# Kernel tuning notes

Measured on AMD Instinct MI355X. Metric: run time of the kernel, lower is better.

Reference implementation:

```python
import jax, jax.numpy as jnp
import numpy as np

VOCAB = 50000
EMB = 300
HID = 1024
MAXLEN = 128
BATCH = 256
M2 = 512


def _xavier(k, shape):
    lim = np.sqrt(6.0 / (shape[0] + shape[-1]))
    return jax.random.uniform(k, shape, jnp.float32, -lim, lim)


def setup_inputs() -> dict:
    key = jax.random.key(0)
    ks = jax.random.split(key, 16)
    return {
        "input1": jax.random.randint(ks[0], (BATCH, MAXLEN), 0, VOCAB, dtype=jnp.int32),
        "input2": jax.random.randint(ks[1], (BATCH, MAXLEN), 0, VOCAB, dtype=jnp.int32),
        "seqlen1": jax.random.randint(ks[2], (BATCH,), 1, MAXLEN + 1, dtype=jnp.int32),
        "seqlen2": jax.random.randint(ks[3], (BATCH,), 1, MAXLEN + 1, dtype=jnp.int32),
        "embeddings": jax.random.normal(ks[4], (VOCAB, EMB), jnp.float32) * 0.1,
        "lstm_kernel": _xavier(ks[5], (EMB + HID, 4 * HID)),
        "lstm_bias": jnp.zeros((4 * HID,), jnp.float32),
        "c1_init": _xavier(ks[6], (BATCH, HID)),
        "h1_init": _xavier(ks[7], (BATCH, HID)),
        "c2_init": _xavier(ks[8], (BATCH, HID)),
        "h2_init": _xavier(ks[9], (BATCH, HID)),
        "W_h": _xavier(ks[10], (HID + 1, HID + 1)),
        "W1": _xavier(ks[11], (3 * (HID + 1) + 1 + BATCH, M2)),
        "b1": _xavier(ks[12], (1, M2)),
        "W2": _xavier(ks[13], (M2, 2)),
        "b2": _xavier(ks[14], (1, 2)),
    }


def _lstm_last_state(x, seqlen, c0, h0, kernel, bias):
    # TF BasicLSTMCell: gates in order i, j, f, o; forget_bias=1.0.
    # dynamic_rnn(sequence_length=...) freezes state past each row's seqlen.
    E = x.shape[-1]
    Wx, Wh = kernel[:E], kernel[E:]
    xg = jnp.einsum('bte,eg->btg', x, Wx) + bias  # [B,T,4H], input proj hoisted out of scan
    T = x.shape[1]

    def step(carry, inputs):
        c, h = carry
        xg_t, t = inputs
        g = xg_t + h @ Wh
        i, j, f, o = jnp.split(g, 4, axis=-1)
        c_new = jax.nn.sigmoid(f + 1.0) * c + jax.nn.sigmoid(i) * jnp.tanh(j)
        h_new = jnp.tanh(c_new) * jax.nn.sigmoid(o)
        valid = (t < seqlen)[:, None]
        return (jnp.where(valid, c_new, c), jnp.where(valid, h_new, h)), None

    (c, h), _ = jax.lax.scan(step, (c0, h0), (jnp.swapaxes(xg, 0, 1), jnp.arange(T)))
    return h


def reference(input1, input2, seqlen1, seqlen2, embeddings, lstm_kernel, lstm_bias,
              c1_init, h1_init, c2_init, h2_init, W_h, W1, b1, W2, b2):
    x1 = embeddings[input1]  # [B,T,E]
    x2 = embeddings[input2]
    h1 = _lstm_last_state(x1, seqlen1, c1_init, h1_init, lstm_kernel, lstm_bias)
    h2 = _lstm_last_state(x2, seqlen2, c2_init, h2_init, lstm_kernel, lstm_bias)
    len1 = (seqlen1.astype(jnp.float32) / float(MAXLEN))[:, None]
    len2 = (seqlen2.astype(jnp.float32) / float(MAXLEN))[:, None]
    h1 = jnp.concatenate([h1, len1], axis=1)  # [B,H+1]
    h2 = jnp.concatenate([h2, len2], axis=1)
    h_dist = jnp.sum(jnp.square(h1 - h2), axis=1, keepdims=True)  # [B,1]
    h_mul = h1 * h2                                               # [B,H+1]
    h_interaction = (h1 @ W_h) @ h2.T                             # [B,B] bilinear block
    h_combined = jnp.concatenate([h1, h2, h_dist, h_mul, h_interaction], axis=1)
    e1 = jax.nn.relu(h_combined @ W1 + b1)  # dropout keep_prob=1 at inference -> identity
    return e1 @ W2 + b2  # [B,2] logits
```

## Files before the change

kernel.cpp:

```cpp
#include <hip/hip_runtime.h>
#include <hip/hip_bf16.h>

typedef __bf16 bf16;
typedef __bf16 bf16x8 __attribute__((ext_vector_type(8)));
typedef float f32x4 __attribute__((ext_vector_type(4)));

#define N_ROWS   512
#define HID      1024
#define KX       320
#define KTOT     1344
#define NSTEPS   128
#define EMB_D    300
#define HC_W     3332

#define WBT_OFF   0UL
#define XB_OFF    11010048UL
#define HB_OFF    52953088UL
#define BIASP_OFF 55050240UL
#define CB_OFF    55066624UL
#define HC_OFF    11010048UL
#define H2T_OFF   14422016UL
#define T1A_OFF   15471616UL
#define T1B_OFF   16521216UL
#define E1A_OFF   17570816UL
#define E1B_OFF   18095104UL


__device__ __forceinline__ float sigm(float x) { return 1.f / (1.f + __expf(-x)); }
__device__ __forceinline__ float tanh_fast(float x) {
  float xc = fminf(fmaxf(x, -15.f), 15.f);
  float e = __expf(2.f * xc);
  return (e - 1.f) / (e + 1.f);
}

__device__ __forceinline__ void lds_barrier() {
  asm volatile("s_waitcnt lgkmcnt(0)" ::: "memory");
  __builtin_amdgcn_sched_barrier(0);
  __builtin_amdgcn_s_barrier();
  __builtin_amdgcn_sched_barrier(0);
}

__global__ void pack_wbt(const float* __restrict__ lk, bf16* __restrict__ wbt) {
  __shared__ float sh[64][65];
  const int px = blockIdx.x;
  const int k0 = blockIdx.y * 64;
  const int t = threadIdx.x;
  {
    const int kk = t >> 2, g = t & 3;
    const int k = k0 + kk;
    const bool valid = (k < KX) ? (k < EMB_D) : true;
    const int src = (k < KX) ? k : (k - 20);
    const float* base = lk + (size_t)src * 4096 + g * 1024 + px * 16;
#pragma unroll
    for (int c4 = 0; c4 < 4; ++c4) {
      float4 v = valid ? *reinterpret_cast<const float4*>(base + c4 * 4)
                       : float4{0.f, 0.f, 0.f, 0.f};
      sh[kk][g * 16 + c4 * 4 + 0] = v.x;
      sh[kk][g * 16 + c4 * 4 + 1] = v.y;
      sh[kk][g * 16 + c4 * 4 + 2] = v.z;
      sh[kk][g * 16 + c4 * 4 + 3] = v.w;
    }
  }
  __syncthreads();
  {
    const int pl = t >> 2, kq = (t & 3) * 16;
    bf16 ov[16];
#pragma unroll
    for (int j = 0; j < 16; ++j) ov[j] = (bf16)sh[kq + j][pl];
    bf16* dst = wbt + (size_t)(px * 64 + pl) * KTOT + k0 + kq;
#pragma unroll
    for (int j = 0; j < 2; ++j)
      *reinterpret_cast<bf16x8*>(dst + j * 8) =
          *reinterpret_cast<const bf16x8*>(&ov[j * 8]);
  }
}

__global__ void pack_xb(const int* __restrict__ in1, const int* __restrict__ in2,
                        const float* __restrict__ emb, bf16* __restrict__ xb) {
  int r = blockIdx.x;
  int t = blockIdx.y * 8 + threadIdx.x / 40;
  int e8 = threadIdx.x % 40;
  int tok = (r < 256) ? in1[r * 128 + t] : in2[(r - 256) * 128 + t];
  const float* er = emb + (size_t)tok * EMB_D + e8 * 8;
  bf16x8 v;
  if (e8 < 37) {
#pragma unroll
    for (int i = 0; i < 8; ++i) v[i] = (bf16)er[i];
  } else {
#pragma unroll
    for (int i = 0; i < 8; ++i) {
      int e = e8 * 8 + i;
      v[i] = (e < EMB_D) ? (bf16)er[i] : (bf16)0.f;
    }
  }
  *reinterpret_cast<bf16x8*>(&xb[((size_t)t * N_ROWS + r) * KX + e8 * 8]) = v;
}

__global__ void pack_misc(const float* __restrict__ h1i, const float* __restrict__ h2i,
                          const float* __restrict__ c1i, const float* __restrict__ c2i,
                          const float* __restrict__ bias, bf16* __restrict__ hb0,
                          float* __restrict__ biasp, float* __restrict__ Cb) {
  int idx = blockIdx.x * 256 + threadIdx.x;
  if (idx < N_ROWS * HID) {
    int r = idx >> 10, k = idx & 1023;
    float v = (r < 256) ? h1i[(size_t)r * HID + k] : h2i[(size_t)(r - 256) * HID + k];
    hb0[idx] = (bf16)v;
    float cv = (r < 256) ? c1i[(size_t)r * HID + k] : c2i[(size_t)(r - 256) * HID + k];
    Cb[idx] = cv;
  }
  if (idx < 4096) {
    int cb = idx >> 6, g = (idx >> 4) & 3, c = idx & 15;
    biasp[idx] = bias[g * HID + cb * 16 + c];
  }
}

__launch_bounds__(256, 2)
__global__ void lstm_step(const bf16* __restrict__ xb, const bf16* __restrict__ wbt,
                          bf16* __restrict__ hb, const float* __restrict__ biasp,
                          float* __restrict__ Cb, const int* __restrict__ s1,
                          const int* __restrict__ s2, int t) {
  __shared__ bf16 As[2][128][64];
  __shared__ bf16 Bs[2][64][64];
  const int tid = threadIdx.x;
  const int wave = tid >> 6;
  const int lane = tid & 63;
  const int lrow = lane & 15;
  const int hi = lane >> 4;
  const int l7 = lane & 7;
  const int bid = blockIdx.x;
  const int rb = bid >> 6;
  const int cb = bid & 63;
  const int r0 = rb * 128;

  const int cellabs = cb * 16 + lrow;

  int slen[2][4];
#pragma unroll
  for (int mi = 0; mi < 2; ++mi)
#pragma unroll
    for (int q = 0; q < 4; ++q) {
      int rr = r0 + wave * 32 + mi * 16 + hi * 4 + q;
      slen[mi][q] = (rr < 256) ? s1[rr] : s2[rr - 256];
    }

  float creg[2][4];
#pragma unroll
  for (int mi = 0; mi < 2; ++mi)
#pragma unroll
    for (int q = 0; q < 4; ++q) {
      int rr = r0 + wave * 32 + mi * 16 + hi * 4 + q;
      creg[mi][q] = Cb[(size_t)rr * HID + cellabs];
    }

  float bv[4];
#pragma unroll
  for (int ni = 0; ni < 4; ++ni)
    bv[ni] = biasp[cb * 64 + ni * 16 + lrow];

  const int a_r = tid >> 1, a_cb = (tid & 1) * 4;
  const int b_r = tid >> 2, b_cb = (tid & 3) * 2;

  const bf16* xt = xb + (size_t)t * N_ROWS * KX;
  const bf16* hc0 = hb + ((size_t)(t & 1) << 19);

  bf16x8 ra[4], rbv2[2];
  auto issue_loads = [&](int nkc) {
    const bf16* asrc = (nkc < 5)
        ? (xt + (size_t)(r0 + a_r) * KX + nkc * 64 + a_cb * 8)
        : (hc0 + ((size_t)(r0 + a_r) << 10) + (nkc * 64 - KX) + a_cb * 8);
#pragma unroll
    for (int q = 0; q < 4; ++q)
      ra[q] = *reinterpret_cast<const bf16x8*>(asrc + q * 8);
    const bf16* bsrc = wbt + (size_t)(cb * 64 + b_r) * KTOT + nkc * 64 + b_cb * 8;
#pragma unroll
    for (int q = 0; q < 2; ++q)
      rbv2[q] = *reinterpret_cast<const bf16x8*>(bsrc + q * 8);
  };
  auto stage_to = [&](int buf) {
#pragma unroll
    for (int q = 0; q < 4; ++q)
      *reinterpret_cast<bf16x8*>(&As[buf][a_r][((a_cb + q) ^ (a_r & 7)) << 3]) = ra[q];
#pragma unroll
    for (int q = 0; q < 2; ++q)
      *reinterpret_cast<bf16x8*>(&Bs[buf][b_r][((b_cb + q) ^ (b_r & 7)) << 3]) = rbv2[q];
  };

  issue_loads(0);
  stage_to(0);
  issue_loads(1);
  __syncthreads();
  int db = 0;

  f32x4 acc[2][4];
#pragma unroll
  for (int mi = 0; mi < 2; ++mi)
#pragma unroll
    for (int ni = 0; ni < 4; ++ni)
      acc[mi][ni] = f32x4{bv[ni], bv[ni], bv[ni], bv[ni]};

  for (int kc = 0; kc < 21; ++kc) {
    if (kc < 20) stage_to(db ^ 1);
    {
      int nkc = kc + 2;
      if (nkc <= 20) issue_loads(nkc);
    }
#pragma unroll
    for (int ks = 0; ks < 2; ++ks) {
      const int cs = (((ks << 2) | hi) ^ l7) << 3;
      bf16x8 af[2], bfv[4];
#pragma unroll
      for (int mi = 0; mi < 2; ++mi)
        af[mi] = *reinterpret_cast<const bf16x8*>(
            &As[db][wave * 32 + mi * 16 + lrow][cs]);
#pragma unroll
      for (int ni = 0; ni < 4; ++ni)
        bfv[ni] = *reinterpret_cast<const bf16x8*>(&Bs[db][ni * 16 + lrow][cs]);
#pragma unroll
      for (int mi = 0; mi < 2; ++mi)
#pragma unroll
        for (int ni = 0; ni < 4; ++ni)
          acc[mi][ni] = __builtin_amdgcn_mfma_f32_16x16x32_bf16(
              af[mi], bfv[ni], acc[mi][ni], 0, 0, 0);
    }
    lds_barrier();
    db ^= 1;
  }

  {
    const bf16* hc = hc0;
    bf16* hnb = hb + (((size_t)(t & 1) << 19) ^ ((size_t)1 << 19));
#pragma unroll
    for (int mi = 0; mi < 2; ++mi)
#pragma unroll
      for (int q = 0; q < 4; ++q) {
        float ig = acc[mi][0][q];
        float jg = acc[mi][1][q];
        float fg = acc[mi][2][q];
        float og = acc[mi][3][q];
        float cn = sigm(fg + 1.f) * creg[mi][q] + sigm(ig) * tanh_fast(jg);
        float hv = tanh_fast(cn) * sigm(og);
        int rr = r0 + wave * 32 + mi * 16 + hi * 4 + q;
        size_t off = ((size_t)rr << 10) + cellabs;
        float ho;
        if (t < slen[mi][q]) {
          Cb[off] = cn;
          ho = hv;
        } else {
          ho = (float)hc[off];
        }
        hnb[off] = (bf16)ho;
      }
  }
}

__global__ void feat_kernel(const bf16* __restrict__ hb0, const int* __restrict__ s1,
                            const int* __restrict__ s2, float* __restrict__ HC,
                            float* __restrict__ H2T) {
  int a = blockIdx.x;
  int tid = threadIdx.x;
  __shared__ float red[256];
  const bf16* h1r = hb0 + (size_t)a * HID;
  const bf16* h2r = hb0 + (size_t)(a + 256) * HID;
  float l1 = (float)s1[a] * (1.f / 128.f);
  float l2 = (float)s2[a] * (1.f / 128.f);
  float dacc = 0.f;
  for (int k = tid; k < 1025; k += 256) {
    float v1 = (k < HID) ? (float)h1r[k] : l1;
    float v2 = (k < HID) ? (float)h2r[k] : l2;
    HC[(size_t)a * HC_W + k] = v1;
    HC[(size_t)a * HC_W + 1025 + k] = v2;
    HC[(size_t)a * HC_W + 2051 + k] = v1 * v2;
    H2T[(size_t)k * 256 + a] = v2;
    float d = v1 - v2;
    dacc += d * d;
  }
  red[tid] = dacc;
  __syncthreads();
  for (int s = 128; s > 0; s >>= 1) {
    if (tid < s) red[tid] += red[tid + s];
    __syncthreads();
  }
  if (tid == 0) HC[(size_t)a * HC_W + 2050] = red[0];
}

__global__ void t1_kernel(const float* __restrict__ HC, const float* __restrict__ Wh,
                          float* __restrict__ T1a, float* __restrict__ T1b) {
  int j = blockIdx.x * 256 + threadIdx.x;
  int a0 = blockIdx.y * 2;
  int z = blockIdx.z;
  const int k0 = z ? 513 : 0;
  const int kn = z ? 512 : 513;
  __shared__ float sh[2][513];
  for (int idx = threadIdx.x; idx < 2 * kn; idx += 256) {
    int r = (idx >= kn) ? 1 : 0;
    int k = idx - r * kn;
    sh[r][k] = HC[(size_t)(a0 + r) * HC_W + k0 + k];
  }
  __syncthreads();
  if (j < 1025) {
    float acc0 = 0.f, acc1 = 0.f;
    for (int k = 0; k < kn; ++k) {
      float w = Wh[(size_t)(k0 + k) * 1025 + j];
      acc0 += sh[0][k] * w;
      acc1 += sh[1][k] * w;
    }
    float* T1 = z ? T1b : T1a;
    T1[(size_t)a0 * 1025 + j] = acc0;
    T1[(size_t)(a0 + 1) * 1025 + j] = acc1;
  }
}

__global__ void inter_kernel(const float* __restrict__ T1a, const float* __restrict__ T1b,
                             const float* __restrict__ H2T, float* __restrict__ HC) {
  int a = blockIdx.x;
  int b = threadIdx.x;
  __shared__ float sT[1025];
  for (int k = threadIdx.x; k < 1025; k += 256)
    sT[k] = T1a[(size_t)a * 1025 + k] + T1b[(size_t)a * 1025 + k];
  __syncthreads();
  float acc = 0.f;
  for (int k = 0; k < 1025; ++k)
    acc += sT[k] * H2T[(size_t)k * 256 + b];
  HC[(size_t)a * HC_W + 3076 + b] = acc;
}

__global__ void e1_kernel(const float* __restrict__ HC, const float* __restrict__ W1,
                          float* __restrict__ E1a, float* __restrict__ E1b) {
  int a0 = blockIdx.x * 2;
  int j = blockIdx.y * 256 + threadIdx.x;
  int z = blockIdx.z;
  const int k0 = z * 1666;
  __shared__ float sh[2][1666];
  for (int idx = threadIdx.x; idx < 2 * 1666; idx += 256) {
    int r = (idx >= 1666) ? 1 : 0;
    int k = idx - r * 1666;
    sh[r][k] = HC[(size_t)(a0 + r) * HC_W + k0 + k];
  }
  __syncthreads();
  float acc0 = 0.f, acc1 = 0.f;
  for (int k = 0; k < 1666; ++k) {
    float w = W1[(size_t)(k0 + k) * 512 + j];
    acc0 += sh[0][k] * w;
    acc1 += sh[1][k] * w;
  }
  float* E1 = z ? E1b : E1a;
  E1[(size_t)a0 * 512 + j] = acc0;
  E1[(size_t)(a0 + 1) * 512 + j] = acc1;
}

__global__ void out_kernel(const float* __restrict__ E1a, const float* __restrict__ E1b,
                           const float* __restrict__ b1, const float* __restrict__ W2,
                           const float* __restrict__ b2, float* __restrict__ out) {
  int a = blockIdx.x;
  int tid = threadIdx.x;
  __shared__ float red0[256], red1[256];
  size_t i0 = (size_t)a * 512 + tid;
  size_t i1 = i0 + 256;
  float v0 = fmaxf(E1a[i0] + E1b[i0] + b1[tid], 0.f);
  float v1 = fmaxf(E1a[i1] + E1b[i1] + b1[tid + 256], 0.f);
  float a0 = v0 * W2[2 * tid] + v1 * W2[2 * (tid + 256)];
  float a1 = v0 * W2[2 * tid + 1] + v1 * W2[2 * (tid + 256) + 1];
  red0[tid] = a0;
  red1[tid] = a1;
  __syncthreads();
  for (int s = 128; s > 0; s >>= 1) {
    if (tid < s) { red0[tid] += red0[tid + s]; red1[tid] += red1[tid + s]; }
    __syncthreads();
  }
  if (tid == 0) {
    out[2 * a] = red0[0] + b2[0];
    out[2 * a + 1] = red1[0] + b2[1];
  }
}

extern "C" void kernel_launch(void* const* d_in, const int* in_sizes, int n_in,
                              void* d_out, int out_size, void* d_ws, size_t ws_size,
                              hipStream_t stream) {
  const int*   input1 = (const int*)d_in[0];
  const int*   input2 = (const int*)d_in[1];
  const int*   seql1  = (const int*)d_in[2];
  const int*   seql2  = (const int*)d_in[3];
  const float* emb    = (const float*)d_in[4];
  const float* lk     = (const float*)d_in[5];
  const float* lbias  = (const float*)d_in[6];
  const float* c1i    = (const float*)d_in[7];
  const float* h1i    = (const float*)d_in[8];
  const float* c2i    = (const float*)d_in[9];
  const float* h2i    = (const float*)d_in[10];
  const float* W_h    = (const float*)d_in[11];
  const float* W1     = (const float*)d_in[12];
  const float* b1     = (const float*)d_in[13];
  const float* W2     = (const float*)d_in[14];
  const float* b2     = (const float*)d_in[15];

  char* ws = (char*)d_ws;
  bf16*     WbT   = (bf16*)(ws + WBT_OFF);
  bf16*     Xb    = (bf16*)(ws + XB_OFF);
  bf16*     Hb    = (bf16*)(ws + HB_OFF);
  float*    biasp = (float*)(ws + BIASP_OFF);
  float*    Cb    = (float*)(ws + CB_OFF);
  float*    HC    = (float*)(ws + HC_OFF);
  float*    H2T   = (float*)(ws + H2T_OFF);
  float*    T1a   = (float*)(ws + T1A_OFF);
  float*    T1b   = (float*)(ws + T1B_OFF);
  float*    E1a   = (float*)(ws + E1A_OFF);
  float*    E1b   = (float*)(ws + E1B_OFF);

  pack_wbt<<<dim3(64, 21), 256, 0, stream>>>(lk, WbT);
  pack_xb<<<dim3(512, 16), 320, 0, stream>>>(input1, input2, emb, Xb);
  pack_misc<<<2048, 256, 0, stream>>>(h1i, h2i, c1i, c2i, lbias, Hb, biasp, Cb);

  for (int t = 0; t < NSTEPS; ++t)
    lstm_step<<<256, 256, 0, stream>>>(Xb, WbT, Hb, biasp, Cb, seql1, seql2, t);

  feat_kernel<<<256, 256, 0, stream>>>(Hb, seql1, seql2, HC, H2T);
  t1_kernel<<<dim3(5, 128, 2), 256, 0, stream>>>(HC, W_h, T1a, T1b);
  inter_kernel<<<256, 256, 0, stream>>>(T1a, T1b, H2T, HC);
  e1_kernel<<<dim3(128, 2, 2), 256, 0, stream>>>(HC, W1, E1a, E1b);
  out_kernel<<<256, 256, 0, stream>>>(E1a, E1b, b1, W2, b2, (float*)d_out);
}
```

Measured before the change: 2.386 ms.

## Deepen LSTM step prefetch to two register stages and split e1 reduction four ways

```diff
diff --git a/kernel.cpp b/kernel.cpp
--- a/kernel.cpp
+++ b/kernel.cpp
@@ -22,8 +22,7 @@
 #define H2T_OFF   14422016UL
 #define T1A_OFF   15471616UL
 #define T1B_OFF   16521216UL
-#define E1A_OFF   17570816UL
-#define E1B_OFF   18095104UL
+#define E1P_OFF   17570816UL
 
 
 __device__ __forceinline__ float sigm(float x) { return 1.f / (1.f + __expf(-x)); }
@@ -114,7 +113,7 @@
   }
 }
 
-__launch_bounds__(256, 2)
+__launch_bounds__(256, 1)
 __global__ void lstm_step(const bf16* __restrict__ xb, const bf16* __restrict__ wbt,
                           bf16* __restrict__ hb, const float* __restrict__ biasp,
                           float* __restrict__ Cb, const int* __restrict__ s1,
@@ -163,8 +162,10 @@
   const bf16* xt = xb + (size_t)t * N_ROWS * KX;
   const bf16* hc0 = hb + ((size_t)(t & 1) << 19);
 
-  bf16x8 ra[4], rbv2[2];
-  auto issue_loads = [&](int nkc) {
+  bf16x8 raA[4], rbA[2], raB[4], rbB[2];
+
+  auto issue_into = [&](bf16x8 (&ra)[4], bf16x8 (&rb2)[2], int nkc) {
+    if (nkc > 20) return;
     const bf16* asrc = (nkc < 5)
         ? (xt + (size_t)(r0 + a_r) * KX + nkc * 64 + a_cb * 8)
         : (hc0 + ((size_t)(r0 + a_r) << 10) + (nkc * 64 - KX) + a_cb * 8);
@@ -174,22 +175,16 @@
     const bf16* bsrc = wbt + (size_t)(cb * 64 + b_r) * KTOT + nkc * 64 + b_cb * 8;
 #pragma unroll
     for (int q = 0; q < 2; ++q)
-      rbv2[q] = *reinterpret_cast<const bf16x8*>(bsrc + q * 8);
+      rb2[q] = *reinterpret_cast<const bf16x8*>(bsrc + q * 8);
   };
-  auto stage_to = [&](int buf) {
+  auto stage_from = [&](bf16x8 (&ra)[4], bf16x8 (&rb2)[2], int buf) {
 #pragma unroll
     for (int q = 0; q < 4; ++q)
       *reinterpret_cast<bf16x8*>(&As[buf][a_r][((a_cb + q) ^ (a_r & 7)) << 3]) = ra[q];
 #pragma unroll
     for (int q = 0; q < 2; ++q)
-      *reinterpret_cast<bf16x8*>(&Bs[buf][b_r][((b_cb + q) ^ (b_r & 7)) << 3]) = rbv2[q];
+      *reinterpret_cast<bf16x8*>(&Bs[buf][b_r][((b_cb + q) ^ (b_r & 7)) << 3]) = rb2[q];
   };
-
-  issue_loads(0);
-  stage_to(0);
-  issue_loads(1);
-  __syncthreads();
-  int db = 0;
 
   f32x4 acc[2][4];
 #pragma unroll
@@ -198,12 +193,7 @@
     for (int ni = 0; ni < 4; ++ni)
       acc[mi][ni] = f32x4{bv[ni], bv[ni], bv[ni], bv[ni]};
 
-  for (int kc = 0; kc < 21; ++kc) {
-    if (kc < 20) stage_to(db ^ 1);
-    {
-      int nkc = kc + 2;
-      if (nkc <= 20) issue_loads(nkc);
-    }
+  auto compute = [&](int buf) {
 #pragma unroll
     for (int ks = 0; ks < 2; ++ks) {
       const int cs = (((ks << 2) | hi) ^ l7) << 3;
@@ -211,10 +201,10 @@
 #pragma unroll
       for (int mi = 0; mi < 2; ++mi)
         af[mi] = *reinterpret_cast<const bf16x8*>(
-            &As[db][wave * 32 + mi * 16 + lrow][cs]);
+            &As[buf][wave * 32 + mi * 16 + lrow][cs]);
 #pragma unroll
       for (int ni = 0; ni < 4; ++ni)
-        bfv[ni] = *reinterpret_cast<const bf16x8*>(&Bs[db][ni * 16 + lrow][cs]);
+        bfv[ni] = *reinterpret_cast<const bf16x8*>(&Bs[buf][ni * 16 + lrow][cs]);
 #pragma unroll
       for (int mi = 0; mi < 2; ++mi)
 #pragma unroll
@@ -222,9 +212,29 @@
           acc[mi][ni] = __builtin_amdgcn_mfma_f32_16x16x32_bf16(
               af[mi], bfv[ni], acc[mi][ni], 0, 0, 0);
     }
+  };
+
+  issue_into(raA, rbA, 0);
+  stage_from(raA, rbA, 0);
+  issue_into(raB, rbB, 1);
+  issue_into(raA, rbA, 2);
+  __syncthreads();
+  int db = 0;
+
+  for (int i = 0; i < 10; ++i) {
+    const int kc = 2 * i;
+    stage_from(raB, rbB, db ^ 1);
+    issue_into(raB, rbB, kc + 3);
+    compute(db);
     lds_barrier();
     db ^= 1;
-  }
+    stage_from(raA, rbA, db ^ 1);
+    issue_into(raA, rbA, kc + 4);
+    compute(db);
+    lds_barrier();
+    db ^= 1;
+  }
+  compute(db);
 
   {
     const bf16* hc = hc0;
@@ -325,39 +335,42 @@
 }
 
 __global__ void e1_kernel(const float* __restrict__ HC, const float* __restrict__ W1,
-                          float* __restrict__ E1a, float* __restrict__ E1b) {
+                          float* __restrict__ E1p) {
   int a0 = blockIdx.x * 2;
   int j = blockIdx.y * 256 + threadIdx.x;
   int z = blockIdx.z;
-  const int k0 = z * 1666;
-  __shared__ float sh[2][1666];
-  for (int idx = threadIdx.x; idx < 2 * 1666; idx += 256) {
-    int r = (idx >= 1666) ? 1 : 0;
-    int k = idx - r * 1666;
+  const int k0 = z * 833;
+  __shared__ float sh[2][833];
+  for (int idx = threadIdx.x; idx < 2 * 833; idx += 256) {
+    int r = (idx >= 833) ? 1 : 0;
+    int k = idx - r * 833;
     sh[r][k] = HC[(size_t)(a0 + r) * HC_W + k0 + k];
   }
   __syncthreads();
   float acc0 = 0.f, acc1 = 0.f;
-  for (int k = 0; k < 1666; ++k) {
+  for (int k = 0; k < 833; ++k) {
     float w = W1[(size_t)(k0 + k) * 512 + j];
     acc0 += sh[0][k] * w;
     acc1 += sh[1][k] * w;
   }
-  float* E1 = z ? E1b : E1a;
+  float* E1 = E1p + (size_t)z * 256 * 512;
   E1[(size_t)a0 * 512 + j] = acc0;
   E1[(size_t)(a0 + 1) * 512 + j] = acc1;
 }
 
-__global__ void out_kernel(const float* __restrict__ E1a, const float* __restrict__ E1b,
+__global__ void out_kernel(const float* __restrict__ E1p,
                            const float* __restrict__ b1, const float* __restrict__ W2,
                            const float* __restrict__ b2, float* __restrict__ out) {
   int a = blockIdx.x;
   int tid = threadIdx.x;
   __shared__ float red0[256], red1[256];
+  const size_t zs = (size_t)256 * 512;
   size_t i0 = (size_t)a * 512 + tid;
   size_t i1 = i0 + 256;
-  float v0 = fmaxf(E1a[i0] + E1b[i0] + b1[tid], 0.f);
-  float v1 = fmaxf(E1a[i1] + E1b[i1] + b1[tid + 256], 0.f);
+  float s0 = E1p[i0] + E1p[i0 + zs] + E1p[i0 + 2 * zs] + E1p[i0 + 3 * zs];
+  float s1 = E1p[i1] + E1p[i1 + zs] + E1p[i1 + 2 * zs] + E1p[i1 + 3 * zs];
+  float v0 = fmaxf(s0 + b1[tid], 0.f);
+  float v1 = fmaxf(s1 + b1[tid + 256], 0.f);
   float a0 = v0 * W2[2 * tid] + v1 * W2[2 * (tid + 256)];
   float a1 = v0 * W2[2 * tid + 1] + v1 * W2[2 * (tid + 256) + 1];
   red0[tid] = a0;
@@ -403,8 +416,7 @@
   float*    H2T   = (float*)(ws + H2T_OFF);
   float*    T1a   = (float*)(ws + T1A_OFF);
   float*    T1b   = (float*)(ws + T1B_OFF);
-  float*    E1a   = (float*)(ws + E1A_OFF);
-  float*    E1b   = (float*)(ws + E1B_OFF);
+  float*    E1p   = (float*)(ws + E1P_OFF);
 
   pack_wbt<<<dim3(64, 21), 256, 0, stream>>>(lk, WbT);
   pack_xb<<<dim3(512, 16), 320, 0, stream>>>(input1, input2, emb, Xb);
@@ -416,6 +428,6 @@
   feat_kernel<<<256, 256, 0, stream>>>(Hb, seql1, seql2, HC, H2T);
   t1_kernel<<<dim3(5, 128, 2), 256, 0, stream>>>(HC, W_h, T1a, T1b);
   inter_kernel<<<256, 256, 0, stream>>>(T1a, T1b, H2T, HC);
-  e1_kernel<<<dim3(128, 2, 2), 256, 0, stream>>>(HC, W1, E1a, E1b);
-  out_kernel<<<256, 256, 0, stream>>>(E1a, E1b, b1, W2, b2, (float*)d_out);
-}
+  e1_kernel<<<dim3(128, 2, 4), 256, 0, stream>>>(HC, W1, E1p);
+  out_kernel<<<256, 256, 0, stream>>>(E1p, b1, W2, b2, (float*)d_out);
+}
```

Result: no change. 2.408 ms (+0.9%).
